# Optimization experiments

Hardware: AMD Instinct MI355X
Metric: run time of the kernel (lower is better)

## Reference

```python
import jax, jax.numpy as jnp
import numpy as np

NSIDE = 128
NPIX = 12 * NSIDE * NSIDE          # HEALPix pixel count, nested ordering
WIN = 16                           # window = 4x4 nested child block (w=1)
SHIFT = WIN // 2
EPS = 1e-5


def _ln(x, g, b):
    mu = x.mean(-1, keepdims=True)
    var = ((x - mu) ** 2).mean(-1, keepdims=True)
    return (x - mu) * jax.lax.rsqrt(var + EPS) * g + b


def _window_attn(x, wq, bq, wp, bp, n_heads):
    B, N, C = x.shape
    D = C // n_heads
    nw = N // WIN
    qkv = (x @ wq + bq).reshape(B, nw, WIN, 3, n_heads, D)
    q, k, v = jnp.moveaxis(qkv, 3, 0)
    q = jnp.swapaxes(q, 2, 3)
    k = jnp.swapaxes(k, 2, 3)
    v = jnp.swapaxes(v, 2, 3)
    scores = jnp.einsum('bwhqd,bwhkd->bwhqk', q, k) * (D ** -0.5)
    attn = jax.nn.softmax(scores, axis=-1)
    out = jnp.einsum('bwhqk,bwhkd->bwhqd', attn, v)
    out = jnp.swapaxes(out, 2, 3).reshape(B, N, C)
    return out @ wp + bp


def _transformer_block(x, p, shift, n_heads):
    if shift:
        x = jnp.roll(x, -SHIFT, axis=1)          # cyclic shift along nested index
    x = x + _window_attn(_ln(x, p['ln1_g'], p['ln1_b']),
                         p['w_qkv'], p['b_qkv'], p['w_proj'], p['b_proj'], n_heads)
    h = _ln(x, p['ln2_g'], p['ln2_b'])
    x = x + jax.nn.gelu(h @ p['w_mlp1'] + p['b_mlp1'], approximate=False) @ p['w_mlp2'] + p['b_mlp2']
    if shift:
        x = jnp.roll(x, SHIFT, axis=1)
    return x


def _forward(x, w_ff1, b_ff1, ln1_g, ln1_b, w_qkv, b_qkv, w_proj, b_proj,
             ln2_g, ln2_b, w_mlp1, b_mlp1, w_mlp2, b_mlp2, w_ff2, b_ff2,
             n_heads=4):
    residual = x
    h = jax.nn.gelu(x @ w_ff1 + b_ff1, approximate=False)
    for i, shift in enumerate((False, True)):
        p = dict(ln1_g=ln1_g[i], ln1_b=ln1_b[i], w_qkv=w_qkv[i], b_qkv=b_qkv[i],
                 w_proj=w_proj[i], b_proj=b_proj[i], ln2_g=ln2_g[i], ln2_b=ln2_b[i],
                 w_mlp1=w_mlp1[i], b_mlp1=b_mlp1[i], w_mlp2=w_mlp2[i], b_mlp2=b_mlp2[i])
        h = _transformer_block(h, p, shift, n_heads)
    return residual + h @ w_ff2 + b_ff2


def setup_inputs() -> dict:
    key = jax.random.key(0)
    ks = jax.random.split(key, 8)
    F, C, M = 64, 128, 512  # node_feat_dim, node_hidden_dim, mlp hidden
    s = 0.02
    return {
        'x': jax.random.normal(ks[0], (1, NPIX, F), jnp.float32),
        'w_ff1': jax.random.normal(ks[1], (F, C), jnp.float32) * s,
        'b_ff1': jnp.zeros((C,), jnp.float32),
        'ln1_g': jnp.ones((2, C), jnp.float32),
        'ln1_b': jnp.zeros((2, C), jnp.float32),
        'w_qkv': jax.random.normal(ks[2], (2, C, 3 * C), jnp.float32) * s,
        'b_qkv': jnp.zeros((2, 3 * C), jnp.float32),
        'w_proj': jax.random.normal(ks[3], (2, C, C), jnp.float32) * s,
        'b_proj': jnp.zeros((2, C), jnp.float32),
        'ln2_g': jnp.ones((2, C), jnp.float32),
        'ln2_b': jnp.zeros((2, C), jnp.float32),
        'w_mlp1': jax.random.normal(ks[4], (2, C, M), jnp.float32) * s,
        'b_mlp1': jnp.zeros((2, M), jnp.float32),
        'w_mlp2': jax.random.normal(ks[5], (2, M, C), jnp.float32) * s,
        'b_mlp2': jnp.zeros((2, C), jnp.float32),
        'w_ff2': jax.random.normal(ks[6], (C, F), jnp.float32) * s,
        'b_ff2': jnp.zeros((F,), jnp.float32),
    }


def reference(x, w_ff1, b_ff1, ln1_g, ln1_b, w_qkv, b_qkv, w_proj, b_proj,
              ln2_g, ln2_b, w_mlp1, b_mlp1, w_mlp2, b_mlp2, w_ff2, b_ff2):
    return _forward(x, w_ff1, b_ff1, ln1_g, ln1_b, w_qkv, b_qkv, w_proj, b_proj,
                    ln2_g, ln2_b, w_mlp1, b_mlp1, w_mlp2, b_mlp2, w_ff2, b_ff2)
```

## Files before the change

kernel.cpp:

```cpp
#include <hip/hip_runtime.h>
#include <hip/hip_bf16.h>
#include <math.h>

#define NPIX 196608
#define SCALE_Q 0.17677669529663687f

typedef __attribute__((ext_vector_type(4))) float f32x4;
typedef __attribute__((ext_vector_type(8))) short short8;
typedef __attribute__((ext_vector_type(4))) short short4v;
typedef __hip_bfloat16 bf16;

__device__ __forceinline__ float gelu_f(float x) {
    float yy = 1.5957691216057308f * (x + 0.044715f * x * x * x);
    float e = __expf(yy);
    return x - x * __builtin_amdgcn_rcpf(e + 1.0f);
}

__device__ __forceinline__ short bfbits(float f) {
    bf16 h = __float2bfloat16(f);
    return *reinterpret_cast<short*>(&h);
}

__device__ __forceinline__ short8 ldsA(const bf16* buf, int row, int el) {
    return *reinterpret_cast<const short8*>(buf + row * 128 + (el ^ ((row & 7) << 3)));
}
__device__ __forceinline__ short8 ldsA64(const bf16* buf, int row, int el) {
    return *reinterpret_cast<const short8*>(buf + row * 64 + (el ^ ((row & 7) << 3)));
}
__device__ __forceinline__ short8 gld8(const bf16* p) {
    return *reinterpret_cast<const short8*>(p);
}

__global__ __launch_bounds__(256) void k_convert(
    const float* __restrict__ wff1, const float* __restrict__ wqkv,
    const float* __restrict__ wproj, const float* __restrict__ wmlp1,
    const float* __restrict__ wmlp2, const float* __restrict__ wff2,
    bf16* __restrict__ dst)
{
    int gid = blockIdx.x * 256 + threadIdx.x;
    if (gid < 8192) {
        int n = gid >> 6, k = gid & 63;
        dst[gid] = __float2bfloat16(wff1[k * 128 + n]);
    } else if (gid < 106496) {
        int r = gid - 8192; int l = r / 49152; r -= l * 49152;
        int n = r >> 7, k = r & 127;
        dst[gid] = __float2bfloat16(wqkv[l * 49152 + k * 384 + n]);
    } else if (gid < 139264) {
        int r = gid - 106496; int l = r / 16384; r -= l * 16384;
        int n = r >> 7, k = r & 127;
        dst[gid] = __float2bfloat16(wproj[l * 16384 + k * 128 + n]);
    } else if (gid < 270336) {
        int r = gid - 139264; int l = r >> 16; r &= 65535;
        int n = r >> 7, k = r & 127;
        dst[gid] = __float2bfloat16(wmlp1[l * 65536 + k * 512 + n]);
    } else if (gid < 401408) {
        int r = gid - 270336; int l = r >> 16; r &= 65535;
        int n = r >> 9, k = r & 511;
        dst[gid] = __float2bfloat16(wmlp2[l * 65536 + k * 128 + n]);
    } else if (gid < 409600) {
        int r = gid - 401408;
        int n = r >> 7, k = r & 127;
        dst[gid] = __float2bfloat16(wff2[k * 64 + n]);
    }
}

template <int OFFSET, int MODE>
__global__ __launch_bounds__(256, 3) void k_block(
    const float* __restrict__ x, float* __restrict__ h,
    const bf16* __restrict__ wf1t, const float* __restrict__ bf1,
    const float* __restrict__ g1, const float* __restrict__ be1,
    const bf16* __restrict__ wqt, const float* __restrict__ bq,
    const bf16* __restrict__ wpt, const float* __restrict__ bp,
    const float* __restrict__ g2, const float* __restrict__ be2,
    const bf16* __restrict__ w1t, const float* __restrict__ b1,
    const bf16* __restrict__ w2t, const float* __restrict__ b2,
    const bf16* __restrict__ wf2t, const float* __restrict__ bf2,
    float* __restrict__ out)
{
    __shared__ __align__(16) bf16 bufA[8192];
    __shared__ __align__(16) bf16 bufB[8192];
    __shared__ __align__(16) bf16 bufC[8192];
    const int tid = threadIdx.x, base = blockIdx.x * 64;
    const int wid = tid >> 6, lrow = tid & 15, lgrp = (tid >> 4) & 3;
    const int cb0 = wid * 32;

    f32x4 hraw[2][4];

    if (MODE == 0) {
        short8 wf1[2][2];
#pragma unroll
        for (int nt = 0; nt < 2; ++nt)
#pragma unroll
            for (int kk = 0; kk < 2; ++kk)
                wf1[nt][kk] = gld8(wf1t + (size_t)(cb0 + nt * 16 + lrow) * 64 + kk * 32 + lgrp * 8);
        {
            int row = tid >> 2, q = tid & 3;
#pragma unroll
            for (int s = 0; s < 2; ++s) {
                int gg = q + s * 4;
                const float4* src = reinterpret_cast<const float4*>(x + (size_t)(base + row) * 64 + gg * 8);
                float4 v0 = src[0], v1 = src[1];
                short8 w;
                w[0] = bfbits(v0.x); w[1] = bfbits(v0.y); w[2] = bfbits(v0.z); w[3] = bfbits(v0.w);
                w[4] = bfbits(v1.x); w[5] = bfbits(v1.y); w[6] = bfbits(v1.z); w[7] = bfbits(v1.w);
                *reinterpret_cast<short8*>(&bufC[row * 64 + ((gg * 8) ^ ((row & 7) << 3))]) = w;
            }
        }
        __syncthreads();
        short8 xb1[4][2];
#pragma unroll
        for (int tt = 0; tt < 4; ++tt)
#pragma unroll
            for (int kk = 0; kk < 2; ++kk)
                xb1[tt][kk] = ldsA64(bufC, tt * 16 + lrow, kk * 32 + lgrp * 8);
        __syncthreads();
#pragma unroll
        for (int nt = 0; nt < 2; ++nt) {
            float4 bv = *reinterpret_cast<const float4*>(bf1 + cb0 + nt * 16 + lgrp * 4);
#pragma unroll
            for (int tt = 0; tt < 4; ++tt) {
                f32x4 d = {0.f, 0.f, 0.f, 0.f};
#pragma unroll
                for (int kk = 0; kk < 2; ++kk)
                    d = __builtin_amdgcn_mfma_f32_16x16x32_bf16(wf1[nt][kk], xb1[tt][kk], d, 0, 0, 0);
                f32x4 r;
                r[0] = gelu_f(d[0] + bv.x); r[1] = gelu_f(d[1] + bv.y);
                r[2] = gelu_f(d[2] + bv.z); r[3] = gelu_f(d[3] + bv.w);
                hraw[nt][tt] = r;
            }
        }
    } else {
#pragma unroll
        for (int nt = 0; nt < 2; ++nt)
#pragma unroll
            for (int tt = 0; tt < 4; ++tt) {
                int tok = base + OFFSET + tt * 16 + lrow; if (tok >= NPIX) tok -= NPIX;
                float4 hv = *reinterpret_cast<const float4*>(h + (size_t)tok * 128 + cb0 + nt * 16 + lgrp * 4);
                f32x4 r; r[0] = hv.x; r[1] = hv.y; r[2] = hv.z; r[3] = hv.w;
                hraw[nt][tt] = r;
            }
        __syncthreads();
    }

    float2* ws = reinterpret_cast<float2*>(bufC);
#pragma unroll
    for (int tt = 0; tt < 4; ++tt) {
        float s = 0.f, q = 0.f;
#pragma unroll
        for (int nt = 0; nt < 2; ++nt)
#pragma unroll
            for (int i = 0; i < 4; ++i) { float v = hraw[nt][tt][i]; s += v; q += v * v; }
        s += __shfl_xor(s, 16, 64); s += __shfl_xor(s, 32, 64);
        q += __shfl_xor(q, 16, 64); q += __shfl_xor(q, 32, 64);
        if (lgrp == 0) { float2 t2; t2.x = s; t2.y = q; ws[wid * 64 + tt * 16 + lrow] = t2; }
    }
    __syncthreads();
    {
        float mu[4], rstd[4];
#pragma unroll
        for (int tt = 0; tt < 4; ++tt) {
            float s = 0.f, q = 0.f;
#pragma unroll
            for (int w = 0; w < 4; ++w) {
                float2 t2 = ws[w * 64 + tt * 16 + lrow];
                s += t2.x; q += t2.y;
            }
            float m = s * (1.f / 128.f);
            mu[tt] = m;
            rstd[tt] = rsqrtf(q * (1.f / 128.f) - m * m + 1e-5f);
        }
        float4 gv[2], bev[2];
#pragma unroll
        for (int nt = 0; nt < 2; ++nt) {
            gv[nt]  = *reinterpret_cast<const float4*>(g1 + cb0 + nt * 16 + lgrp * 4);
            bev[nt] = *reinterpret_cast<const float4*>(be1 + cb0 + nt * 16 + lgrp * 4);
        }
#pragma unroll
        for (int nt = 0; nt < 2; ++nt)
#pragma unroll
            for (int tt = 0; tt < 4; ++tt) {
                short4v pk;
                pk[0] = bfbits((hraw[nt][tt][0] - mu[tt]) * rstd[tt] * gv[nt].x + bev[nt].x);
                pk[1] = bfbits((hraw[nt][tt][1] - mu[tt]) * rstd[tt] * gv[nt].y + bev[nt].y);
                pk[2] = bfbits((hraw[nt][tt][2] - mu[tt]) * rstd[tt] * gv[nt].z + bev[nt].z);
                pk[3] = bfbits((hraw[nt][tt][3] - mu[tt]) * rstd[tt] * gv[nt].w + bev[nt].w);
                int row = tt * 16 + lrow;
                int c = cb0 + nt * 16 + lgrp * 4;
                *reinterpret_cast<short4v*>(&bufA[row * 128 + (c ^ ((row & 7) << 3))]) = pk;
            }
    }

    const int qc = wid * 96;
    short8 wq0[2][4], wq1[2][4];
#pragma unroll
    for (int j = 0; j < 2; ++j)
#pragma unroll
        for (int kk = 0; kk < 4; ++kk)
            wq0[j][kk] = gld8(wqt + (size_t)(qc + j * 16 + lrow) * 128 + kk * 32 + lgrp * 8);
    __syncthreads();

    short8 xb[4][4];
#pragma unroll
    for (int tt = 0; tt < 4; ++tt)
#pragma unroll
        for (int kk = 0; kk < 4; ++kk)
            xb[tt][kk] = ldsA(bufA, tt * 16 + lrow, kk * 32 + lgrp * 8);
    __syncthreads();

#define QKV_TILE(WF, NB)                                                            \
    {                                                                               \
        const int cb = qc + (NB) * 16;                                              \
        float4 bqv = *reinterpret_cast<const float4*>(bq + cb + lgrp * 4);          \
        _Pragma("unroll")                                                           \
        for (int tt = 0; tt < 4; ++tt) {                                            \
            f32x4 d = {0.f, 0.f, 0.f, 0.f};                                         \
            _Pragma("unroll")                                                       \
            for (int kk = 0; kk < 4; ++kk)                                          \
                d = __builtin_amdgcn_mfma_f32_16x16x32_bf16(WF[kk], xb[tt][kk], d, 0, 0, 0); \
            int row = tt * 16 + lrow;                                               \
            if (cb < 128) {                                                         \
                int c = cb + lgrp * 4;                                              \
                short4v pk;                                                         \
                pk[0] = bfbits((d[0] + bqv.x) * SCALE_Q); pk[1] = bfbits((d[1] + bqv.y) * SCALE_Q); \
                pk[2] = bfbits((d[2] + bqv.z) * SCALE_Q); pk[3] = bfbits((d[3] + bqv.w) * SCALE_Q); \
                *reinterpret_cast<short4v*>(&bufA[row * 128 + (c ^ ((row & 7) << 3))]) = pk; \
            } else if (cb < 256) {                                                  \
                int c = cb - 128 + lgrp * 4;                                        \
                short4v pk;                                                         \
                pk[0] = bfbits(d[0] + bqv.x); pk[1] = bfbits(d[1] + bqv.y);         \
                pk[2] = bfbits(d[2] + bqv.z); pk[3] = bfbits(d[3] + bqv.w);         \
                *reinterpret_cast<short4v*>(&bufB[row * 128 + (c ^ ((row & 7) << 3))]) = pk; \
            } else {                                                                \
                int db = cb - 256 + lgrp * 4;                                       \
                bufC[tt * 2048 + (db + 0) * 16 + lrow] = __float2bfloat16(d[0] + bqv.x); \
                bufC[tt * 2048 + (db + 1) * 16 + lrow] = __float2bfloat16(d[1] + bqv.y); \
                bufC[tt * 2048 + (db + 2) * 16 + lrow] = __float2bfloat16(d[2] + bqv.z); \
                bufC[tt * 2048 + (db + 3) * 16 + lrow] = __float2bfloat16(d[3] + bqv.w); \
            }                                                                       \
        }                                                                           \
    }

#pragma unroll
    for (int j = 0; j < 2; ++j)
#pragma unroll
        for (int kk = 0; kk < 4; ++kk)
            wq1[j][kk] = gld8(wqt + (size_t)(qc + (j + 2) * 16 + lrow) * 128 + kk * 32 + lgrp * 8);
    QKV_TILE(wq0[0], 0) QKV_TILE(wq0[1], 1)
#pragma unroll
    for (int j = 0; j < 2; ++j)
#pragma unroll
        for (int kk = 0; kk < 4; ++kk)
            wq0[j][kk] = gld8(wqt + (size_t)(qc + (j + 4) * 16 + lrow) * 128 + kk * 32 + lgrp * 8);
    QKV_TILE(wq1[0], 2) QKV_TILE(wq1[1], 3)
    QKV_TILE(wq0[0], 4) QKV_TILE(wq0[1], 5)
    __syncthreads();

    short8 wfp[2][4];
#pragma unroll
    for (int nt = 0; nt < 2; ++nt)
#pragma unroll
        for (int kk = 0; kk < 4; ++kk)
            wfp[nt][kk] = gld8(wpt + (size_t)(cb0 + nt * 16 + lrow) * 128 + kk * 32 + lgrp * 8);

    float p[4][4];
#pragma unroll
    for (int hh = 0; hh < 4; ++hh) {
        short8 aq = ldsA(bufA, wid * 16 + lrow, hh * 32 + lgrp * 8);
        short8 bk = ldsA(bufB, wid * 16 + lrow, hh * 32 + lgrp * 8);
        f32x4 z = {0.f, 0.f, 0.f, 0.f};
        f32x4 s = __builtin_amdgcn_mfma_f32_16x16x32_bf16(aq, bk, z, 0, 0, 0);
#pragma unroll
        for (int i = 0; i < 4; ++i) {
            float m_ = s[i];
            m_ = fmaxf(m_, __shfl_xor(m_, 1, 64));
            m_ = fmaxf(m_, __shfl_xor(m_, 2, 64));
            m_ = fmaxf(m_, __shfl_xor(m_, 4, 64));
            m_ = fmaxf(m_, __shfl_xor(m_, 8, 64));
            float e = __expf(s[i] - m_);
            float sum = e;
            sum += __shfl_xor(sum, 1, 64);
            sum += __shfl_xor(sum, 2, 64);
            sum += __shfl_xor(sum, 4, 64);
            sum += __shfl_xor(sum, 8, 64);
            p[hh][i] = e * __builtin_amdgcn_rcpf(sum);
        }
    }
    bf16* pl = bufB + wid * 2048;
#pragma unroll
    for (int hh = 0; hh < 4; ++hh)
#pragma unroll
        for (int i = 0; i < 4; ++i)
            pl[hh * 256 + (lgrp * 4 + i) * 16 + lrow] = __float2bfloat16(p[hh][i]);

    short8 z8 = {0, 0, 0, 0, 0, 0, 0, 0};
#pragma unroll
    for (int dt = 0; dt < 8; ++dt) {
        int hh = dt >> 1;
        short8 av = z8, bv = z8;
        if (lgrp < 2) {
            av = *reinterpret_cast<const short8*>(&bufC[wid * 2048 + (dt * 16 + lrow) * 16 + lgrp * 8]);
            bv = *reinterpret_cast<const short8*>(&pl[hh * 256 + lrow * 16 + lgrp * 8]);
        }
        f32x4 z = {0.f, 0.f, 0.f, 0.f};
        f32x4 o = __builtin_amdgcn_mfma_f32_16x16x32_bf16(av, bv, z, 0, 0, 0);
        int row = wid * 16 + lrow;
        int c = dt * 16 + lgrp * 4;
        short4v pk;
        pk[0] = bfbits(o[0]); pk[1] = bfbits(o[1]); pk[2] = bfbits(o[2]); pk[3] = bfbits(o[3]);
        *reinterpret_cast<short4v*>(&bufA[row * 128 + (c ^ ((row & 7) << 3))]) = pk;
    }
    __syncthreads();

    short8 af[4][4];
#pragma unroll
    for (int tt = 0; tt < 4; ++tt)
#pragma unroll
        for (int kk = 0; kk < 4; ++kk)
            af[tt][kk] = ldsA(bufA, tt * 16 + lrow, kk * 32 + lgrp * 8);
    f32x4 hres[2][4];
#pragma unroll
    for (int nt = 0; nt < 2; ++nt) {
        float4 bpv = *reinterpret_cast<const float4*>(bp + cb0 + nt * 16 + lgrp * 4);
#pragma unroll
        for (int tt = 0; tt < 4; ++tt) {
            f32x4 d = {0.f, 0.f, 0.f, 0.f};
#pragma unroll
            for (int kk = 0; kk < 4; ++kk)
                d = __builtin_amdgcn_mfma_f32_16x16x32_bf16(wfp[nt][kk], af[tt][kk], d, 0, 0, 0);
            f32x4 r = hraw[nt][tt];
            r[0] += bpv.x + d[0]; r[1] += bpv.y + d[1];
            r[2] += bpv.z + d[2]; r[3] += bpv.w + d[3];
            hres[nt][tt] = r;
        }
    }

#pragma unroll
    for (int tt = 0; tt < 4; ++tt) {
        float s = 0.f, q = 0.f;
#pragma unroll
        for (int nt = 0; nt < 2; ++nt)
#pragma unroll
            for (int i = 0; i < 4; ++i) { float v = hres[nt][tt][i]; s += v; q += v * v; }
        s += __shfl_xor(s, 16, 64); s += __shfl_xor(s, 32, 64);
        q += __shfl_xor(q, 16, 64); q += __shfl_xor(q, 32, 64);
        if (lgrp == 0) { float2 t2; t2.x = s; t2.y = q; ws[wid * 64 + tt * 16 + lrow] = t2; }
    }
    __syncthreads();
    short8 w1f[2][2][4];
    {
        float mu[4], rstd[4];
#pragma unroll
        for (int tt = 0; tt < 4; ++tt) {
            float s = 0.f, q = 0.f;
#pragma unroll
            for (int w = 0; w < 4; ++w) {
                float2 t2 = ws[w * 64 + tt * 16 + lrow];
                s += t2.x; q += t2.y;
            }
            float m = s * (1.f / 128.f);
            mu[tt] = m;
            rstd[tt] = rsqrtf(q * (1.f / 128.f) - m * m + 1e-5f);
        }
        float4 gv[2], bev[2];
#pragma unroll
        for (int nt = 0; nt < 2; ++nt) {
            gv[nt]  = *reinterpret_cast<const float4*>(g2 + cb0 + nt * 16 + lgrp * 4);
            bev[nt] = *reinterpret_cast<const float4*>(be2 + cb0 + nt * 16 + lgrp * 4);
        }
#pragma unroll
        for (int nt = 0; nt < 2; ++nt)
#pragma unroll
            for (int tt = 0; tt < 4; ++tt) {
                short4v pk;
                pk[0] = bfbits((hres[nt][tt][0] - mu[tt]) * rstd[tt] * gv[nt].x + bev[nt].x);
                pk[1] = bfbits((hres[nt][tt][1] - mu[tt]) * rstd[tt] * gv[nt].y + bev[nt].y);
                pk[2] = bfbits((hres[nt][tt][2] - mu[tt]) * rstd[tt] * gv[nt].z + bev[nt].z);
                pk[3] = bfbits((hres[nt][tt][3] - mu[tt]) * rstd[tt] * gv[nt].w + bev[nt].w);
                int row = tt * 16 + lrow;
                int c = cb0 + nt * 16 + lgrp * 4;
                *reinterpret_cast<short4v*>(&bufB[row * 128 + (c ^ ((row & 7) << 3))]) = pk;
            }
    }
#pragma unroll
    for (int nt = 0; nt < 2; ++nt)
#pragma unroll
        for (int kk = 0; kk < 4; ++kk)
            w1f[0][nt][kk] = gld8(w1t + (size_t)(cb0 + nt * 16 + lrow) * 128 + kk * 32 + lgrp * 8);
    __syncthreads();

    f32x4 acc2[2][4];
#pragma unroll
    for (int nt = 0; nt < 2; ++nt)
#pragma unroll
        for (int tt = 0; tt < 4; ++tt) acc2[nt][tt] = (f32x4){0.f, 0.f, 0.f, 0.f};

#pragma unroll
    for (int ch = 0; ch < 4; ++ch) {
        short8 w2f[2][4];
#pragma unroll
        for (int nt = 0; nt < 2; ++nt)
#pragma unroll
            for (int kk = 0; kk < 4; ++kk)
                w2f[nt][kk] = gld8(w2t + (size_t)(cb0 + nt * 16 + lrow) * 512 + ch * 128 + kk * 32 + lgrp * 8);
        float4 b1v[2];
#pragma unroll
        for (int nt = 0; nt < 2; ++nt)
            b1v[nt] = *reinterpret_cast<const float4*>(b1 + ch * 128 + cb0 + nt * 16 + lgrp * 4);
#pragma unroll
        for (int tt = 0; tt < 4; ++tt) {
            short8 xf[4];
#pragma unroll
            for (int kk = 0; kk < 4; ++kk)
                xf[kk] = ldsA(bufB, tt * 16 + lrow, kk * 32 + lgrp * 8);
#pragma unroll
            for (int nt = 0; nt < 2; ++nt) {
                f32x4 d = {0.f, 0.f, 0.f, 0.f};
#pragma unroll
                for (int kk = 0; kk < 4; ++kk)
                    d = __builtin_amdgcn_mfma_f32_16x16x32_bf16(w1f[ch & 1][nt][kk], xf[kk], d, 0, 0, 0);
                short4v pk;
                pk[0] = bfbits(gelu_f(d[0] + b1v[nt].x)); pk[1] = bfbits(gelu_f(d[1] + b1v[nt].y));
                pk[2] = bfbits(gelu_f(d[2] + b1v[nt].z)); pk[3] = bfbits(gelu_f(d[3] + b1v[nt].w));
                int row = tt * 16 + lrow;
                int c = cb0 + nt * 16 + lgrp * 4;
                *reinterpret_cast<short4v*>(&bufA[row * 128 + (c ^ ((row & 7) << 3))]) = pk;
            }
        }
        __syncthreads();
        if (ch < 3) {
#pragma unroll
            for (int nt = 0; nt < 2; ++nt)
#pragma unroll
                for (int kk = 0; kk < 4; ++kk)
                    w1f[(ch + 1) & 1][nt][kk] =
                        gld8(w1t + (size_t)((ch + 1) * 128 + cb0 + nt * 16 + lrow) * 128 + kk * 32 + lgrp * 8);
        }
#pragma unroll
        for (int tt = 0; tt < 4; ++tt) {
            short8 uf[4];
#pragma unroll
            for (int kk = 0; kk < 4; ++kk)
                uf[kk] = ldsA(bufA, tt * 16 + lrow, kk * 32 + lgrp * 8);
#pragma unroll
            for (int nt = 0; nt < 2; ++nt)
#pragma unroll
                for (int kk = 0; kk < 4; ++kk)
                    acc2[nt][tt] = __builtin_amdgcn_mfma_f32_16x16x32_bf16(
                        w2f[nt][kk], uf[kk], acc2[nt][tt], 0, 0, 0);
        }
        __syncthreads();
    }

    if (MODE == 0) {
#pragma unroll
        for (int nt = 0; nt < 2; ++nt) {
            const int n0 = cb0 + nt * 16 + lgrp * 4;
            float4 b2v = *reinterpret_cast<const float4*>(b2 + n0);
#pragma unroll
            for (int tt = 0; tt < 4; ++tt) {
                int tok = base + OFFSET + tt * 16 + lrow; if (tok >= NPIX) tok -= NPIX;
                float4 ov;
                ov.x = hres[nt][tt][0] + b2v.x + acc2[nt][tt][0];
                ov.y = hres[nt][tt][1] + b2v.y + acc2[nt][tt][1];
                ov.z = hres[nt][tt][2] + b2v.z + acc2[nt][tt][2];
                ov.w = hres[nt][tt][3] + b2v.w + acc2[nt][tt][3];
                *reinterpret_cast<float4*>(h + (size_t)tok * 128 + n0) = ov;
            }
        }
    } else {
        short8 wff[4];
#pragma unroll
        for (int kk = 0; kk < 4; ++kk)
            wff[kk] = gld8(wf2t + (size_t)(wid * 16 + lrow) * 128 + kk * 32 + lgrp * 8);
        float4 xv[4];
#pragma unroll
        for (int tt = 0; tt < 4; ++tt) {
            int tok = base + OFFSET + tt * 16 + lrow; if (tok >= NPIX) tok -= NPIX;
            xv[tt] = *reinterpret_cast<const float4*>(x + (size_t)tok * 64 + wid * 16 + lgrp * 4);
        }
#pragma unroll
        for (int nt = 0; nt < 2; ++nt) {
            const int n0 = cb0 + nt * 16 + lgrp * 4;
            float4 b2v = *reinterpret_cast<const float4*>(b2 + n0);
#pragma unroll
            for (int tt = 0; tt < 4; ++tt) {
                short4v pk;
                pk[0] = bfbits(hres[nt][tt][0] + b2v.x + acc2[nt][tt][0]);
                pk[1] = bfbits(hres[nt][tt][1] + b2v.y + acc2[nt][tt][1]);
                pk[2] = bfbits(hres[nt][tt][2] + b2v.z + acc2[nt][tt][2]);
                pk[3] = bfbits(hres[nt][tt][3] + b2v.w + acc2[nt][tt][3]);
                int row = tt * 16 + lrow;
                int c = cb0 + nt * 16 + lgrp * 4;
                *reinterpret_cast<short4v*>(&bufB[row * 128 + (c ^ ((row & 7) << 3))]) = pk;
            }
        }
        __syncthreads();
        float4 bfv = *reinterpret_cast<const float4*>(bf2 + wid * 16 + lgrp * 4);
#pragma unroll
        for (int tt = 0; tt < 4; ++tt) {
            short8 bfr[4];
#pragma unroll
            for (int kk = 0; kk < 4; ++kk)
                bfr[kk] = ldsA(bufB, tt * 16 + lrow, kk * 32 + lgrp * 8);
            f32x4 d = {0.f, 0.f, 0.f, 0.f};
#pragma unroll
            for (int kk = 0; kk < 4; ++kk)
                d = __builtin_amdgcn_mfma_f32_16x16x32_bf16(wff[kk], bfr[kk], d, 0, 0, 0);
            int tok = base + OFFSET + tt * 16 + lrow; if (tok >= NPIX) tok -= NPIX;
            float4 ov;
            ov.x = xv[tt].x + bfv.x + d[0]; ov.y = xv[tt].y + bfv.y + d[1];
            ov.z = xv[tt].z + bfv.z + d[2]; ov.w = xv[tt].w + bfv.w + d[3];
            *reinterpret_cast<float4*>(out + (size_t)tok * 64 + wid * 16 + lgrp * 4) = ov;
        }
    }
#undef QKV_TILE
}

extern "C" void kernel_launch(void* const* d_in, const int* in_sizes, int n_in,
                              void* d_out, int out_size, void* d_ws, size_t ws_size,
                              hipStream_t stream) {
    (void)in_sizes; (void)n_in; (void)out_size; (void)ws_size;
    const float* x      = (const float*)d_in[0];
    const float* w_ff1  = (const float*)d_in[1];
    const float* b_ff1  = (const float*)d_in[2];
    const float* ln1_g  = (const float*)d_in[3];
    const float* ln1_b  = (const float*)d_in[4];
    const float* w_qkv  = (const float*)d_in[5];
    const float* b_qkv  = (const float*)d_in[6];
    const float* w_proj = (const float*)d_in[7];
    const float* b_proj = (const float*)d_in[8];
    const float* ln2_g  = (const float*)d_in[9];
    const float* ln2_b  = (const float*)d_in[10];
    const float* w_mlp1 = (const float*)d_in[11];
    const float* b_mlp1 = (const float*)d_in[12];
    const float* w_mlp2 = (const float*)d_in[13];
    const float* b_mlp2 = (const float*)d_in[14];
    const float* w_ff2  = (const float*)d_in[15];
    const float* b_ff2  = (const float*)d_in[16];
    float* out = (float*)d_out;

    float* h = (float*)d_ws;
    bf16* wbf = (bf16*)((char*)d_ws + (size_t)NPIX * 128 * 4);
    bf16* ff1t  = wbf;
    bf16* qkvt  = wbf + 8192;
    bf16* projt = wbf + 106496;
    bf16* mlp1t = wbf + 139264;
    bf16* mlp2t = wbf + 270336;
    bf16* ff2t  = wbf + 401408;

    dim3 blk(256);
    k_convert<<<1600, blk, 0, stream>>>(w_ff1, w_qkv, w_proj, w_mlp1, w_mlp2, w_ff2, wbf);

    const int NB = NPIX / 64;
    k_block<0, 0><<<NB, blk, 0, stream>>>(x, h,
        ff1t, b_ff1,
        ln1_g, ln1_b, qkvt, b_qkv, projt, b_proj,
        ln2_g, ln2_b, mlp1t, b_mlp1, mlp2t, b_mlp2,
        ff2t, b_ff2, out);

    k_block<8, 1><<<NB, blk, 0, stream>>>(x, h,
        ff1t, b_ff1,
        ln1_g + 128, ln1_b + 128, qkvt + 49152, b_qkv + 384, projt + 16384, b_proj + 128,
        ln2_g + 128, ln2_b + 128, mlp1t + 65536, b_mlp1 + 512, mlp2t + 65536, b_mlp2 + 128,
        ff2t, b_ff2, out);
}
```

Baseline: 488.0 us.

## Use LDS-only barriers and double-buffer MLP hidden chunks to halve syncs

Replaces __syncthreads with a custom barrier that waits only on LDS/scalar counters (lgkmcnt) rather than on outstanding global loads, so prefetched weight loads can stay in flight across barriers. The MLP chunk loop alternates between two LDS buffers, which removes one barrier per chunk, and an unneeded barrier in the MODE-1 path is dropped. The sched_barrier fences limit compiler reordering, and correctness now depends on the buffer-alternation reasoning being right.

```diff
diff --git a/kernel.cpp b/kernel.cpp
--- a/kernel.cpp
+++ b/kernel.cpp
@@ -29,6 +29,13 @@
 }
 __device__ __forceinline__ short8 gld8(const bf16* p) {
     return *reinterpret_cast<const short8*>(p);
+}
+
+__device__ __forceinline__ void bar_lds() {
+    __builtin_amdgcn_sched_barrier(0);
+    asm volatile("s_waitcnt lgkmcnt(0)" ::: "memory");
+    __builtin_amdgcn_s_barrier();
+    __builtin_amdgcn_sched_barrier(0);
 }
 
 __global__ __launch_bounds__(256) void k_convert(
@@ -106,14 +113,14 @@
                 *reinterpret_cast<short8*>(&bufC[row * 64 + ((gg * 8) ^ ((row & 7) << 3))]) = w;
             }
         }
-        __syncthreads();
+        bar_lds();
         short8 xb1[4][2];
 #pragma unroll
         for (int tt = 0; tt < 4; ++tt)
 #pragma unroll
             for (int kk = 0; kk < 2; ++kk)
                 xb1[tt][kk] = ldsA64(bufC, tt * 16 + lrow, kk * 32 + lgrp * 8);
-        __syncthreads();
+        bar_lds();
 #pragma unroll
         for (int nt = 0; nt < 2; ++nt) {
             float4 bv = *reinterpret_cast<const float4*>(bf1 + cb0 + nt * 16 + lgrp * 4);
@@ -139,7 +146,6 @@
                 f32x4 r; r[0] = hv.x; r[1] = hv.y; r[2] = hv.z; r[3] = hv.w;
                 hraw[nt][tt] = r;
             }
-        __syncthreads();
     }
 
     float2* ws = reinterpret_cast<float2*>(bufC);
@@ -154,7 +160,7 @@
         q += __shfl_xor(q, 16, 64); q += __shfl_xor(q, 32, 64);
         if (lgrp == 0) { float2 t2; t2.x = s; t2.y = q; ws[wid * 64 + tt * 16 + lrow] = t2; }
     }
-    __syncthreads();
+    bar_lds();
     {
         float mu[4], rstd[4];
 #pragma unroll
@@ -197,7 +203,7 @@
 #pragma unroll
         for (int kk = 0; kk < 4; ++kk)
             wq0[j][kk] = gld8(wqt + (size_t)(qc + j * 16 + lrow) * 128 + kk * 32 + lgrp * 8);
-    __syncthreads();
+    bar_lds();
 
     short8 xb[4][4];
 #pragma unroll
@@ -205,7 +211,7 @@
 #pragma unroll
         for (int kk = 0; kk < 4; ++kk)
             xb[tt][kk] = ldsA(bufA, tt * 16 + lrow, kk * 32 + lgrp * 8);
-    __syncthreads();
+    bar_lds();
 
 #define QKV_TILE(WF, NB)                                                            \
     {                                                                               \
@@ -253,7 +259,7 @@
             wq0[j][kk] = gld8(wqt + (size_t)(qc + (j + 4) * 16 + lrow) * 128 + kk * 32 + lgrp * 8);
     QKV_TILE(wq1[0], 2) QKV_TILE(wq1[1], 3)
     QKV_TILE(wq0[0], 4) QKV_TILE(wq0[1], 5)
-    __syncthreads();
+    bar_lds();
 
     short8 wfp[2][4];
 #pragma unroll
@@ -309,7 +315,7 @@
         pk[0] = bfbits(o[0]); pk[1] = bfbits(o[1]); pk[2] = bfbits(o[2]); pk[3] = bfbits(o[3]);
         *reinterpret_cast<short4v*>(&bufA[row * 128 + (c ^ ((row & 7) << 3))]) = pk;
     }
-    __syncthreads();
+    bar_lds();
 
     short8 af[4][4];
 #pragma unroll
@@ -345,7 +351,7 @@
         q += __shfl_xor(q, 16, 64); q += __shfl_xor(q, 32, 64);
         if (lgrp == 0) { float2 t2; t2.x = s; t2.y = q; ws[wid * 64 + tt * 16 + lrow] = t2; }
     }
-    __syncthreads();
+    bar_lds();
     short8 w1f[2][2][4];
     {
         float mu[4], rstd[4];
@@ -386,7 +392,7 @@
 #pragma unroll
         for (int kk = 0; kk < 4; ++kk)
             w1f[0][nt][kk] = gld8(w1t + (size_t)(cb0 + nt * 16 + lrow) * 128 + kk * 32 + lgrp * 8);
-    __syncthreads();
+    bar_lds();
 
     f32x4 acc2[2][4];
 #pragma unroll
@@ -396,6 +402,7 @@
 
 #pragma unroll
     for (int ch = 0; ch < 4; ++ch) {
+        bf16* UB = (ch & 1) ? bufC : bufA;
         short8 w2f[2][4];
 #pragma unroll
         for (int nt = 0; nt < 2; ++nt)
@@ -423,10 +430,9 @@
                 pk[2] = bfbits(gelu_f(d[2] + b1v[nt].z)); pk[3] = bfbits(gelu_f(d[3] + b1v[nt].w));
                 int row = tt * 16 + lrow;
                 int c = cb0 + nt * 16 + lgrp * 4;
-                *reinterpret_cast<short4v*>(&bufA[row * 128 + (c ^ ((row & 7) << 3))]) = pk;
-            }
-        }
-        __syncthreads();
+                *reinterpret_cast<short4v*>(&UB[row * 128 + (c ^ ((row & 7) << 3))]) = pk;
+            }
+        }
         if (ch < 3) {
 #pragma unroll
             for (int nt = 0; nt < 2; ++nt)
@@ -435,12 +441,13 @@
                     w1f[(ch + 1) & 1][nt][kk] =
                         gld8(w1t + (size_t)((ch + 1) * 128 + cb0 + nt * 16 + lrow) * 128 + kk * 32 + lgrp * 8);
         }
+        bar_lds();
 #pragma unroll
         for (int tt = 0; tt < 4; ++tt) {
             short8 uf[4];
 #pragma unroll
             for (int kk = 0; kk < 4; ++kk)
-                uf[kk] = ldsA(bufA, tt * 16 + lrow, kk * 32 + lgrp * 8);
+                uf[kk] = ldsA(UB, tt * 16 + lrow, kk * 32 + lgrp * 8);
 #pragma unroll
             for (int nt = 0; nt < 2; ++nt)
 #pragma unroll
@@ -448,7 +455,6 @@
                     acc2[nt][tt] = __builtin_amdgcn_mfma_f32_16x16x32_bf16(
                         w2f[nt][kk], uf[kk], acc2[nt][tt], 0, 0, 0);
         }
-        __syncthreads();
     }
 
     if (MODE == 0) {
@@ -478,6 +484,7 @@
             int tok = base + OFFSET + tt * 16 + lrow; if (tok >= NPIX) tok -= NPIX;
             xv[tt] = *reinterpret_cast<const float4*>(x + (size_t)tok * 64 + wid * 16 + lgrp * 4);
         }
+        bar_lds();
 #pragma unroll
         for (int nt = 0; nt < 2; ++nt) {
             const int n0 = cb0 + nt * 16 + lgrp * 4;
@@ -494,7 +501,7 @@
                 *reinterpret_cast<short4v*>(&bufB[row * 128 + (c ^ ((row & 7) << 3))]) = pk;
             }
         }
-        __syncthreads();
+        bar_lds();
         float4 bfv = *reinterpret_cast<const float4*>(bf2 + wid * 16 + lgrp * 4);
 #pragma unroll
         for (int tt = 0; tt < 4; ++tt) {
@@ -548,17 +555,16 @@
     bf16* mlp2t = wbf + 270336;
     bf16* ff2t  = wbf + 401408;
 
-    dim3 blk(256);
-    k_convert<<<1600, blk, 0, stream>>>(w_ff1, w_qkv, w_proj, w_mlp1, w_mlp2, w_ff2, wbf);
+    k_convert<<<1600, dim3(256), 0, stream>>>(w_ff1, w_qkv, w_proj, w_mlp1, w_mlp2, w_ff2, wbf);
 
     const int NB = NPIX / 64;
-    k_block<0, 0><<<NB, blk, 0, stream>>>(x, h,
+    k_block<0, 0><<<NB, dim3(256), 0, stream>>>(x, h,
         ff1t, b_ff1,
         ln1_g, ln1_b, qkvt, b_qkv, projt, b_proj,
         ln2_g, ln2_b, mlp1t, b_mlp1, mlp2t, b_mlp2,
         ff2t, b_ff2, out);
 
-    k_block<8, 1><<<NB, blk, 0, stream>>>(x, h,
+    k_block<8, 1><<<NB, dim3(256), 0, stream>>>(x, h,
         ff1t, b_ff1,
         ln1_g + 128, ln1_b + 128, qkvt + 49152, b_qkv + 384, projt + 16384, b_proj + 128,
         ln2_g + 128, ln2_b + 128, mlp1t + 65536, b_mlp1 + 512, mlp2t + 65536, b_mlp2 + 128,
```

New measurement: 542.4 us. +11.1%, slower.
